# Kernel tuning notes

Measured on AMD Instinct MI355X. Metric: run time of the kernel, lower is better.

## Reference

```python
import jax, jax.numpy as jnp
import numpy as np
from jax import lax

ROUTE_SCALE = 1.0

def setup_inputs() -> dict:
    key = jax.random.key(0)
    k1, k2 = jax.random.split(key)
    B, C, H, Wd = 64, 768, 32, 32
    E = 64
    x = jax.random.normal(k1, (B, C, H, Wd), dtype=jnp.float32)
    W = jax.random.normal(k2, (E, C), dtype=jnp.float32) * 0.02  # nn.Linear-like scale
    b = jnp.zeros((E,), dtype=jnp.float32)
    route_bias = jnp.zeros((E,), dtype=jnp.float32)  # register_buffer 'bias'
    return {"x": x, "W": W, "b": b, "route_bias": route_bias, "topk": 8}

def reference(x, W, b, route_bias, topk):
    # AdaptiveAvgPool2d(1) + Flatten -> global mean over spatial dims: [B, C]
    pooled = jnp.mean(x, axis=(2, 3))
    # Linear(C -> E), then sigmoid
    scores = jax.nn.sigmoid(jnp.einsum('bc,ec->be', pooled, W) + b)  # [B, E]
    original_scores = scores
    biased = scores + route_bias
    # top-k selection on biased scores, gather from original scores
    _, indices = lax.top_k(biased, topk)                      # [B, K] int32
    weights = jnp.take_along_axis(original_scores, indices, axis=-1)  # [B, K]
    weights = weights / jnp.sum(weights, axis=-1, keepdims=True)
    weights = weights * ROUTE_SCALE
    return weights, indices
```

## Files before the change

### kernel.cpp

```cpp
#include <hip/hip_runtime.h>
#include <math.h>

#define B_DIM 64
#define C_DIM 768
#define S_DIM 1024
#define E_DIM 64

__global__ __launch_bounds__(256) void pool_kernel(const float* __restrict__ x,
                                                   float* __restrict__ pooled,
                                                   int nrows) {
    int wave = (int)((blockIdx.x * blockDim.x + threadIdx.x) >> 6);
    int lane = threadIdx.x & 63;
    if (wave >= nrows) return;

    const float4* p = (const float4*)(x + (size_t)wave * S_DIM);
    float s = 0.0f;
#pragma unroll
    for (int k = 0; k < 4; ++k) {
        float4 v = p[k * 64 + lane];
        s += (v.x + v.y) + (v.z + v.w);
    }
#pragma unroll
    for (int off = 1; off < 64; off <<= 1) s += __shfl_xor(s, off);
    if (lane == 0) pooled[wave] = s * (1.0f / (float)S_DIM);
}

__global__ __launch_bounds__(256) void gate_kernel(const float* __restrict__ pooled,
                                                   const float* __restrict__ Wm,
                                                   const float* __restrict__ bvec,
                                                   const float* __restrict__ route_bias,
                                                   int K,
                                                   float* __restrict__ out) {
    __shared__ __align__(16) float s_pool[C_DIM];
    __shared__ float s_scores[E_DIM];

    const int b   = blockIdx.x;
    const int tid = threadIdx.x;

    const float* prow = pooled + (size_t)b * C_DIM;
    for (int i = tid; i < C_DIM; i += 256) s_pool[i] = prow[i];
    __syncthreads();

    const int e = tid >> 2;
    const int q = tid & 3;
    const float4* wrow  = (const float4*)(Wm + (size_t)e * C_DIM + q * 192);
    const float4* prow4 = (const float4*)(s_pool + q * 192);
    float acc = 0.0f;
#pragma unroll 8
    for (int i = 0; i < 48; ++i) {
        float4 wv = wrow[i];
        float4 pv = prow4[i];
        acc += wv.x * pv.x + wv.y * pv.y + wv.z * pv.z + wv.w * pv.w;
    }
    acc += __shfl_xor(acc, 1);
    acc += __shfl_xor(acc, 2);
    if (q == 0) {
        float z = acc + bvec[e];
        s_scores[e] = 1.0f / (1.0f + expf(-z));
    }
    __syncthreads();

    if (tid < 64) {
        const int lane = tid;
        float myval = s_scores[lane] + route_bias[lane];
        int sel_idx = 0;
        bool have_sel = false;

        for (int k = 0; k < K; ++k) {
            float v = myval;
            int   i = lane;
#pragma unroll
            for (int off = 1; off < 64; off <<= 1) {
                float ov = __shfl_xor(v, off);
                int   oi = __shfl_xor(i, off);
                if (ov > v || (ov == v && oi < i)) { v = ov; i = oi; }
            }
            if (lane == k) { sel_idx = i; have_sel = true; }
            if (lane == i) myval = -INFINITY;
        }

        float w = have_sel ? s_scores[sel_idx] : 0.0f;
        float tot = w;
#pragma unroll
        for (int off = 1; off < 64; off <<= 1) tot += __shfl_xor(tot, off);

        if (lane < K) {
            out[(size_t)b * K + lane] = w / tot;
            out[(size_t)B_DIM * K + (size_t)b * K + lane] = (float)sel_idx;
        }
    }
}

extern "C" void kernel_launch(void* const* d_in, const int* in_sizes, int n_in,
                              void* d_out, int out_size, void* d_ws, size_t ws_size,
                              hipStream_t stream) {
    const float* x          = (const float*)d_in[0];
    const float* Wm         = (const float*)d_in[1];
    const float* bvec       = (const float*)d_in[2];
    const float* route_bias = (const float*)d_in[3];
    const int K = out_size / (2 * B_DIM);

    float* pooled = (float*)d_ws;
    float* out    = (float*)d_out;

    const int nrows  = B_DIM * C_DIM;
    const int blocks = (nrows * 64 + 255) / 256;
    pool_kernel<<<blocks, 256, 0, stream>>>(x, pooled, nrows);
    gate_kernel<<<B_DIM, 256, 0, stream>>>(pooled, Wm, bvec, route_bias, K, out);
}
```

Before: 284.0 us.

## Fuse pooling and gating into one kernel with last-block-done counter

Merges the spatial-mean pooling kernel and the gate/top-k kernel into a single launch. Each of 768 blocks pools 64 channels for one batch row, bumps a per-batch atomic counter, and the last finishing block computes the linear, sigmoid and top-k for that row. This removes the second kernel launch and the serialization between kernels, but adds a memset launch, atomics and fences, and drops the grid from 12288 to 768 blocks, which may reduce memory-level parallelism for the 200MB read.

```diff
diff --git a/kernel.cpp b/kernel.cpp
--- a/kernel.cpp
+++ b/kernel.cpp
@@ -5,40 +5,65 @@
 #define C_DIM 768
 #define S_DIM 1024
 #define E_DIM 64
+#define GROUPS 12
+#define CG     64
 
-__global__ __launch_bounds__(256) void pool_kernel(const float* __restrict__ x,
-                                                   float* __restrict__ pooled,
-                                                   int nrows) {
-    int wave = (int)((blockIdx.x * blockDim.x + threadIdx.x) >> 6);
-    int lane = threadIdx.x & 63;
-    if (wave >= nrows) return;
+#define POOL_BYTES (B_DIM * C_DIM * sizeof(float))
 
-    const float4* p = (const float4*)(x + (size_t)wave * S_DIM);
-    float s = 0.0f;
-#pragma unroll
-    for (int k = 0; k < 4; ++k) {
-        float4 v = p[k * 64 + lane];
-        s += (v.x + v.y) + (v.z + v.w);
-    }
-#pragma unroll
-    for (int off = 1; off < 64; off <<= 1) s += __shfl_xor(s, off);
-    if (lane == 0) pooled[wave] = s * (1.0f / (float)S_DIM);
-}
-
-__global__ __launch_bounds__(256) void gate_kernel(const float* __restrict__ pooled,
-                                                   const float* __restrict__ Wm,
-                                                   const float* __restrict__ bvec,
-                                                   const float* __restrict__ route_bias,
-                                                   int K,
-                                                   float* __restrict__ out) {
+__global__ __launch_bounds__(256) void fused_gate(const float* __restrict__ x,
+                                                  const float* __restrict__ Wm,
+                                                  const float* __restrict__ bvec,
+                                                  const float* __restrict__ route_bias,
+                                                  int K,
+                                                  float* __restrict__ ws_pool,
+                                                  int*   __restrict__ ws_cnt,
+                                                  float* __restrict__ out) {
     __shared__ __align__(16) float s_pool[C_DIM];
     __shared__ float s_scores[E_DIM];
+    __shared__ int   s_last;
 
-    const int b   = blockIdx.x;
-    const int tid = threadIdx.x;
+    const int tid  = threadIdx.x;
+    const int wv   = tid >> 6;
+    const int lane = tid & 63;
+    const int b    = blockIdx.x & (B_DIM - 1);
+    const int g    = blockIdx.x >> 6;
 
-    const float* prow = pooled + (size_t)b * C_DIM;
-    for (int i = tid; i < C_DIM; i += 256) s_pool[i] = prow[i];
+    const int c0 = g * CG + wv * 16;
+    const float4* xbase = (const float4*)(x + ((size_t)b * C_DIM + c0) * S_DIM);
+
+#pragma unroll 2
+    for (int i = 0; i < 16; ++i) {
+        const float4* p = xbase + (size_t)i * (S_DIM / 4);
+        float s = 0.0f;
+#pragma unroll
+        for (int k = 0; k < 4; ++k) {
+            float4 v = p[k * 64 + lane];
+            s += (v.x + v.y) + (v.z + v.w);
+        }
+#pragma unroll
+        for (int off = 1; off < 64; off <<= 1) s += __shfl_xor(s, off);
+        if (lane == 0) {
+            __hip_atomic_store(&ws_pool[(size_t)b * C_DIM + c0 + i],
+                               s * (1.0f / (float)S_DIM),
+                               __ATOMIC_RELAXED, __HIP_MEMORY_SCOPE_AGENT);
+        }
+    }
+
+    __syncthreads();
+    if (tid == 0) {
+        __threadfence();
+        int old = __hip_atomic_fetch_add(&ws_cnt[b], 1, __ATOMIC_ACQ_REL,
+                                         __HIP_MEMORY_SCOPE_AGENT);
+        s_last = (old == GROUPS - 1) ? 1 : 0;
+    }
+    __syncthreads();
+    if (!s_last) return;
+
+    __threadfence();
+    const float* prow = ws_pool + (size_t)b * C_DIM;
+    for (int i = tid; i < C_DIM; i += 256)
+        s_pool[i] = __hip_atomic_load(&prow[i], __ATOMIC_RELAXED,
+                                      __HIP_MEMORY_SCOPE_AGENT);
     __syncthreads();
 
     const int e = tid >> 2;
@@ -48,9 +73,9 @@
     float acc = 0.0f;
 #pragma unroll 8
     for (int i = 0; i < 48; ++i) {
-        float4 wv = wrow[i];
-        float4 pv = prow4[i];
-        acc += wv.x * pv.x + wv.y * pv.y + wv.z * pv.z + wv.w * pv.w;
+        float4 wvv = wrow[i];
+        float4 pv  = prow4[i];
+        acc += wvv.x * pv.x + wvv.y * pv.y + wvv.z * pv.z + wvv.w * pv.w;
     }
     acc += __shfl_xor(acc, 1);
     acc += __shfl_xor(acc, 2);
@@ -61,22 +86,22 @@
     __syncthreads();
 
     if (tid < 64) {
-        const int lane = tid;
-        float myval = s_scores[lane] + route_bias[lane];
-        int sel_idx = 0;
+        const int l = tid;
+        float myval = s_scores[l] + route_bias[l];
+        int  sel_idx  = 0;
         bool have_sel = false;
 
         for (int k = 0; k < K; ++k) {
             float v = myval;
-            int   i = lane;
+            int   i = l;
 #pragma unroll
             for (int off = 1; off < 64; off <<= 1) {
                 float ov = __shfl_xor(v, off);
                 int   oi = __shfl_xor(i, off);
                 if (ov > v || (ov == v && oi < i)) { v = ov; i = oi; }
             }
-            if (lane == k) { sel_idx = i; have_sel = true; }
-            if (lane == i) myval = -INFINITY;
+            if (l == k) { sel_idx = i; have_sel = true; }
+            if (l == i) myval = -INFINITY;
         }
 
         float w = have_sel ? s_scores[sel_idx] : 0.0f;
@@ -84,9 +109,9 @@
 #pragma unroll
         for (int off = 1; off < 64; off <<= 1) tot += __shfl_xor(tot, off);
 
-        if (lane < K) {
-            out[(size_t)b * K + lane] = w / tot;
-            out[(size_t)B_DIM * K + (size_t)b * K + lane] = (float)sel_idx;
+        if (l < K) {
+            out[(size_t)b * K + l] = w / tot;
+            out[(size_t)B_DIM * K + (size_t)b * K + l] = (float)sel_idx;
         }
     }
 }
@@ -100,11 +125,12 @@
     const float* route_bias = (const float*)d_in[3];
     const int K = out_size / (2 * B_DIM);
 
-    float* pooled = (float*)d_ws;
-    float* out    = (float*)d_out;
+    float* ws_pool = (float*)d_ws;
+    int*   ws_cnt  = (int*)((char*)d_ws + POOL_BYTES);
+    float* out     = (float*)d_out;
 
-    const int nrows  = B_DIM * C_DIM;
-    const int blocks = (nrows * 64 + 255) / 256;
-    pool_kernel<<<blocks, 256, 0, stream>>>(x, pooled, nrows);
-    gate_kernel<<<B_DIM, 256, 0, stream>>>(pooled, Wm, bvec, route_bias, K, out);
+    hipMemsetAsync(ws_cnt, 0, B_DIM * sizeof(int), stream);
+
+    fused_gate<<<B_DIM * GROUPS, 256, 0, stream>>>(x, Wm, bvec, route_bias, K,
+                                                   ws_pool, ws_cnt, out);
 }
```

New measurement: 344.8 us. 21.4% more time.
